# Performance work log

Hardware: AMD Instinct MI355X
Metric: run time of the kernel (lower is better)

Reference implementation:

```python
import jax, jax.numpy as jnp
import numpy as np

Q_MAX = 127.0  # 8-bit, narrow range [-127, 127] (pytorch-quantization default)


def fake_quant(x, amax):
    """Fake quantization with clipped-STE semantics (matches pytorch-quantization).

    amax may be a scalar (per-tensor) or broadcastable (per-channel). Treated as
    a constant (stop_gradient'd by caller where appropriate).
    """
    amax = jnp.maximum(amax, 1e-12)
    scale = amax / Q_MAX
    xq = jnp.round(jnp.clip(x / scale, -Q_MAX, Q_MAX)) * scale
    xc = jnp.clip(x, -amax, amax)  # identity grad inside range, zero outside
    return xc + jax.lax.stop_gradient(xq - xc)


def quant_conv1x1(x, w, b):
    """QuantConv2d with 1x1 kernel: fake-quant input (per-tensor dynamic max amax)
    and weight (per-output-channel max amax), then conv + bias.
    x: [B,C,H,W], w: [O,C], b: [O]
    """
    a_amax = jax.lax.stop_gradient(jnp.max(jnp.abs(x)))
    xq = fake_quant(x, a_amax)
    w_amax = jax.lax.stop_gradient(jnp.max(jnp.abs(w), axis=1, keepdims=True))
    wq = fake_quant(w, w_amax)
    y = jnp.einsum('bchw,oc->bohw', xq, wq)
    return y + b[None, :, None, None]


def setup_inputs() -> dict:
    key = jax.random.key(0)
    k1, k2, k3, k4 = jax.random.split(key, 4)
    B, C, Cr, H, W = 64, 32, 8, 128, 128
    x = jax.random.normal(k1, (B, C, H, W), dtype=jnp.float32)
    identity = jax.random.normal(k2, (B, C, H, W), dtype=jnp.float32)
    w_reduce = jax.random.normal(k3, (Cr, C), dtype=jnp.float32) * 0.1
    b_reduce = jnp.zeros((Cr,), dtype=jnp.float32)
    w_expand = jax.random.normal(k4, (C, Cr), dtype=jnp.float32) * 0.1
    b_expand = jnp.zeros((C,), dtype=jnp.float32)
    return {"x": x, "identity": identity,
            "w_reduce": w_reduce, "b_reduce": b_reduce,
            "w_expand": w_expand, "b_expand": b_expand}


def reference(x, identity, w_reduce, b_reduce, w_expand, b_expand):
    h = quant_conv1x1(x, w_reduce, b_reduce)      # [B,8,H,W]
    h = h * jax.nn.sigmoid(h)                     # SiLU
    g = quant_conv1x1(h, w_expand, b_expand)      # [B,32,H,W]
    return identity * jax.nn.sigmoid(g)
```

## Files before the change

kernel.cpp:

```cpp
#include <hip/hip_runtime.h>
#include <math.h>

#define QMAX 127.0f
#define CIN 32
#define CR 8
#define HW 16384
#define BATCH 64
#define NPIX (BATCH*HW)
#define NQUAD (NPIX/4)
#define NX (BATCH*CIN*HW)
#define COOP_BLOCKS (NQUAD/256)

#define H_OFF 64
#define WS_NEEDED ((size_t)(H_OFF + (size_t)NPIX * CR) * 4)

__device__ __forceinline__ float fq(float v, float inv_scale, float scale) {
    return rintf(fminf(fmaxf(v * inv_scale, -QMAX), QMAX)) * scale;
}
__device__ __forceinline__ float sigmoidf_(float v) {
    return __builtin_amdgcn_rcpf(1.0f + __expf(-v));
}

__device__ __forceinline__ void grid_bar(unsigned int* __restrict__ cnt,
                                         unsigned int* __restrict__ gen,
                                         unsigned int nb) {
    __syncthreads();
    if (threadIdx.x == 0) {
        unsigned int g = __hip_atomic_load(gen, __ATOMIC_RELAXED, __HIP_MEMORY_SCOPE_AGENT);
        unsigned int a = __hip_atomic_fetch_add(cnt, 1u, __ATOMIC_ACQ_REL, __HIP_MEMORY_SCOPE_AGENT);
        if (a == nb - 1u) {
            __hip_atomic_store(cnt, 0u, __ATOMIC_RELAXED, __HIP_MEMORY_SCOPE_AGENT);
            __hip_atomic_fetch_add(gen, 1u, __ATOMIC_RELEASE, __HIP_MEMORY_SCOPE_AGENT);
        } else {
            while (__hip_atomic_load(gen, __ATOMIC_RELAXED, __HIP_MEMORY_SCOPE_AGENT) == g)
                __builtin_amdgcn_s_sleep(1);
            __builtin_amdgcn_fence(__ATOMIC_ACQUIRE, "agent");
        }
    }
    __syncthreads();
}

__global__ __launch_bounds__(256, 4) void se_fused(const float* __restrict__ x,
                                                   const float* __restrict__ identity,
                                                   const float* __restrict__ wr,
                                                   const float* __restrict__ br,
                                                   const float* __restrict__ we,
                                                   const float* __restrict__ be,
                                                   unsigned int* __restrict__ wsu,
                                                   float* __restrict__ out) {
    int t = threadIdx.x;
    __shared__ float wqr[CR * CIN], wqe[CIN * CR], bsh[CR], besh[CIN], amr[CR], ame[CIN];
    __shared__ float red[4];

    if (t < CR) {
        float mm = 0.f;
        for (int c = 0; c < CIN; c++) mm = fmaxf(mm, fabsf(wr[t * CIN + c]));
        amr[t] = fmaxf(mm, 1e-12f);
        bsh[t] = br[t];
    }
    if (t >= 64 && t < 64 + CIN) {
        int r = t - 64;
        float mm = 0.f;
        for (int c = 0; c < CR; c++) mm = fmaxf(mm, fabsf(we[r * CR + c]));
        ame[r] = fmaxf(mm, 1e-12f);
        besh[r] = be[r];
    }
    __syncthreads();
    {
        float a1 = amr[t >> 5];
        wqr[t] = fq(wr[t], QMAX / a1, a1 * (1.f / QMAX));
        float a2 = ame[t >> 3];
        wqe[t] = fq(we[t], QMAX / a2, a2 * (1.f / QMAX));
    }
    __syncthreads();

    const int tid = blockIdx.x * 256 + t;

    {
        const float4* x4 = (const float4*)x;
        float m = 0.f;
#pragma unroll 8
        for (int i = 0; i < 32; i++) {
            float4 v = x4[tid + i * NQUAD];
            m = fmaxf(m, fmaxf(fmaxf(fabsf(v.x), fabsf(v.y)), fmaxf(fabsf(v.z), fabsf(v.w))));
        }
#pragma unroll
        for (int off = 32; off > 0; off >>= 1) m = fmaxf(m, __shfl_xor(m, off, 64));
        if ((t & 63) == 0) red[t >> 6] = m;
        __syncthreads();
        if (t == 0) {
            m = fmaxf(fmaxf(red[0], red[1]), fmaxf(red[2], red[3]));
            atomicMax(&wsu[0], __float_as_uint(m));
        }
    }
    grid_bar(&wsu[2], &wsu[3], COOP_BLOCKS);

    float a_amax = fmaxf(__uint_as_float(
        __hip_atomic_load(&wsu[0], __ATOMIC_ACQUIRE, __HIP_MEMORY_SCOPE_AGENT)), 1e-12f);
    float ascale = a_amax * (1.f / QMAX), ainv = QMAX / a_amax;
    const int b = tid >> 12;
    const int hw = (tid & 4095) << 2;
    const size_t base = (size_t)b * CIN * HW + hw;
    float h[CR][4];
    {
        float hacc[CR][4];
#pragma unroll
        for (int o = 0; o < CR; o++)
#pragma unroll
            for (int v = 0; v < 4; v++) hacc[o][v] = 0.f;
        const float* xb = x + base;
#pragma unroll
        for (int c = 0; c < CIN; c++) {
            float4 xv = *(const float4*)(xb + (size_t)c * HW);
            float q0 = fq(xv.x, ainv, ascale), q1 = fq(xv.y, ainv, ascale);
            float q2 = fq(xv.z, ainv, ascale), q3 = fq(xv.w, ainv, ascale);
#pragma unroll
            for (int o = 0; o < CR; o++) {
                float w = wqr[o * CIN + c];
                hacc[o][0] += q0 * w; hacc[o][1] += q1 * w;
                hacc[o][2] += q2 * w; hacc[o][3] += q3 * w;
            }
        }
        float m = 0.f;
#pragma unroll
        for (int o = 0; o < CR; o++) {
            float bb = bsh[o];
#pragma unroll
            for (int v = 0; v < 4; v++) {
                float hv = hacc[o][v] + bb;
                hv = hv * sigmoidf_(hv);
                h[o][v] = hv;
                m = fmaxf(m, fabsf(hv));
            }
        }
#pragma unroll
        for (int off = 32; off > 0; off >>= 1) m = fmaxf(m, __shfl_xor(m, off, 64));
        __syncthreads();
        if ((t & 63) == 0) red[t >> 6] = m;
        __syncthreads();
        if (t == 0) {
            m = fmaxf(fmaxf(red[0], red[1]), fmaxf(red[2], red[3]));
            atomicMax(&wsu[1], __float_as_uint(m));
        }
    }
    grid_bar(&wsu[2], &wsu[3], COOP_BLOCKS);

    float h_amax = fmaxf(__uint_as_float(
        __hip_atomic_load(&wsu[1], __ATOMIC_ACQUIRE, __HIP_MEMORY_SCOPE_AGENT)), 1e-12f);
    float hscale = h_amax * (1.f / QMAX), hinv = QMAX / h_amax;
#pragma unroll
    for (int o = 0; o < CR; o++)
#pragma unroll
        for (int v = 0; v < 4; v++) h[o][v] = fq(h[o][v], hinv, hscale);

#pragma unroll 4
    for (int o2 = 0; o2 < CIN; o2++) {
        float g0 = besh[o2], g1 = g0, g2 = g0, g3 = g0;
#pragma unroll
        for (int cr = 0; cr < CR; cr++) {
            float w = wqe[o2 * CR + cr];
            g0 += h[cr][0] * w; g1 += h[cr][1] * w;
            g2 += h[cr][2] * w; g3 += h[cr][3] * w;
        }
        size_t off = base + (size_t)o2 * HW;
        float4 idv = *(const float4*)(identity + off);
        float4 ov;
        ov.x = idv.x * sigmoidf_(g0);
        ov.y = idv.y * sigmoidf_(g1);
        ov.z = idv.z * sigmoidf_(g2);
        ov.w = idv.w * sigmoidf_(g3);
        *(float4*)(out + off) = ov;
    }
}

__global__ __launch_bounds__(256) void k1_xmax(const float4* __restrict__ x4,
                                               unsigned int* __restrict__ wsu) {
    int idx = blockIdx.x * 256 + threadIdx.x;
    float m = 0.f;
#pragma unroll
    for (int i = 0; i < 16; i++) {
        float4 v = x4[idx + i * 524288];
        m = fmaxf(m, fmaxf(fmaxf(fabsf(v.x), fabsf(v.y)), fmaxf(fabsf(v.z), fabsf(v.w))));
    }
#pragma unroll
    for (int off = 32; off > 0; off >>= 1) m = fmaxf(m, __shfl_xor(m, off, 64));
    __shared__ float red[4];
    int t = threadIdx.x;
    if ((t & 63) == 0) red[t >> 6] = m;
    __syncthreads();
    if (t == 0) {
        m = fmaxf(fmaxf(red[0], red[1]), fmaxf(red[2], red[3]));
        atomicMax(&wsu[0], __float_as_uint(m));
    }
}

__global__ __launch_bounds__(256) void k2_hmax(const float* __restrict__ x,
                                               const float* __restrict__ wr,
                                               const float* __restrict__ br,
                                               const unsigned int* __restrict__ wsu,
                                               unsigned int* __restrict__ hmax,
                                               float* __restrict__ hbuf) {
    __shared__ float wq[CR * CIN], bsh[CR], amr[CR];
    int t = threadIdx.x;
    if (t < CR) {
        float mm = 0.f;
        for (int c = 0; c < CIN; c++) mm = fmaxf(mm, fabsf(wr[t * CIN + c]));
        amr[t] = fmaxf(mm, 1e-12f);
        bsh[t] = br[t];
    }
    __syncthreads();
    {
        float amax = amr[t >> 5];
        wq[t] = fq(wr[t], QMAX / amax, amax * (1.f / QMAX));
    }
    __syncthreads();
    float a_amax = fmaxf(__uint_as_float(wsu[0]), 1e-12f);
    float scale = a_amax * (1.f / QMAX), inv_scale = QMAX / a_amax;
    int tid = blockIdx.x * 256 + t;
    int b = tid >> 12;
    int hw = (tid & 4095) << 2;
    const float* xb = x + (size_t)b * CIN * HW + hw;
    float hacc[CR][4];
#pragma unroll
    for (int o = 0; o < CR; o++)
#pragma unroll
        for (int v = 0; v < 4; v++) hacc[o][v] = 0.f;
#pragma unroll
    for (int c = 0; c < CIN; c++) {
        float4 xv = *(const float4*)(xb + (size_t)c * HW);
        float q0 = fq(xv.x, inv_scale, scale), q1 = fq(xv.y, inv_scale, scale);
        float q2 = fq(xv.z, inv_scale, scale), q3 = fq(xv.w, inv_scale, scale);
#pragma unroll
        for (int o = 0; o < CR; o++) {
            float w = wq[o * CIN + c];
            hacc[o][0] += q0 * w; hacc[o][1] += q1 * w;
            hacc[o][2] += q2 * w; hacc[o][3] += q3 * w;
        }
    }
    float m = 0.f;
#pragma unroll
    for (int o = 0; o < CR; o++) {
        float bb = bsh[o];
        float4 hv;
        float* hp = (float*)&hv;
#pragma unroll
        for (int v = 0; v < 4; v++) {
            float h = hacc[o][v] + bb;
            h = h * sigmoidf_(h);
            hp[v] = h;
            m = fmaxf(m, fabsf(h));
        }
        if (hbuf) *(float4*)(hbuf + ((size_t)(b * CR + o)) * HW + hw) = hv;
    }
#pragma unroll
    for (int off = 32; off > 0; off >>= 1) m = fmaxf(m, __shfl_xor(m, off, 64));
    __shared__ float red[4];
    if ((t & 63) == 0) red[t >> 6] = m;
    __syncthreads();
    if (t == 0) {
        m = fmaxf(fmaxf(red[0], red[1]), fmaxf(red[2], red[3]));
        atomicMax(hmax, __float_as_uint(m));
    }
}

__global__ __launch_bounds__(256) void k3_out(const float* __restrict__ hbuf,
                                              const float* __restrict__ identity,
                                              const float* __restrict__ we,
                                              const float* __restrict__ be,
                                              const unsigned int* __restrict__ wsu,
                                              float* __restrict__ out) {
    const int y = blockIdx.y;
    __shared__ float wqe[16 * CR], besh[16], ame[16];
    int t = threadIdx.x;
    if (t < 16) {
        int r = 16 * y + t;
        float mm = 0.f;
        for (int c = 0; c < CR; c++) mm = fmaxf(mm, fabsf(we[r * CR + c]));
        ame[t] = fmaxf(mm, 1e-12f);
        besh[t] = be[r];
    }
    __syncthreads();
    if (t < 128) {
        int r16 = t >> 3;
        float amax = ame[r16];
        wqe[t] = fq(we[(16 * y + r16) * CR + (t & 7)], QMAX / amax, amax * (1.f / QMAX));
    }
    __syncthreads();
    float h_amax = fmaxf(__uint_as_float(wsu[1]), 1e-12f);
    float hscale = h_amax * (1.f / QMAX), hinv = QMAX / h_amax;
    int tid = blockIdx.x * 256 + t;
    int b = tid >> 12;
    int hw = (tid & 4095) << 2;
    size_t base = (size_t)b * CIN * HW + hw;
    float hq[CR][4];
#pragma unroll
    for (int cr = 0; cr < CR; cr++) {
        float4 hv = *(const float4*)(hbuf + ((size_t)(b * CR + cr)) * HW + hw);
        hq[cr][0] = fq(hv.x, hinv, hscale);
        hq[cr][1] = fq(hv.y, hinv, hscale);
        hq[cr][2] = fq(hv.z, hinv, hscale);
        hq[cr][3] = fq(hv.w, hinv, hscale);
    }
#pragma unroll 4
    for (int o = 0; o < 16; o++) {
        float g0 = besh[o], g1 = g0, g2 = g0, g3 = g0;
#pragma unroll
        for (int cr = 0; cr < CR; cr++) {
            float w = wqe[o * CR + cr];
            g0 += hq[cr][0] * w; g1 += hq[cr][1] * w;
            g2 += hq[cr][2] * w; g3 += hq[cr][3] * w;
        }
        size_t off = base + (size_t)(16 * y + o) * HW;
        float4 idv = *(const float4*)(identity + off);
        float4 ov;
        ov.x = idv.x * sigmoidf_(g0);
        ov.y = idv.y * sigmoidf_(g1);
        ov.z = idv.z * sigmoidf_(g2);
        ov.w = idv.w * sigmoidf_(g3);
        *(float4*)(out + off) = ov;
    }
}

__global__ __launch_bounds__(256) void k3_out_rc(const float* __restrict__ x,
                                                 const float* __restrict__ identity,
                                                 const float* __restrict__ wr,
                                                 const float* __restrict__ br,
                                                 const float* __restrict__ we,
                                                 const float* __restrict__ be,
                                                 const unsigned int* __restrict__ wsu,
                                                 float* __restrict__ out) {
    __shared__ float wqr[CR * CIN], wqe[CIN * CR], bsh[CR], besh[CIN], amr[CR], ame[CIN];
    int t = threadIdx.x;
    if (t < CR) {
        float mm = 0.f;
        for (int c = 0; c < CIN; c++) mm = fmaxf(mm, fabsf(wr[t * CIN + c]));
        amr[t] = fmaxf(mm, 1e-12f);
        bsh[t] = br[t];
    }
    if (t >= 64 && t < 64 + CIN) {
        int r = t - 64;
        float mm = 0.f;
        for (int c = 0; c < CR; c++) mm = fmaxf(mm, fabsf(we[r * CR + c]));
        ame[r] = fmaxf(mm, 1e-12f);
        besh[r] = be[r];
    }
    __syncthreads();
    {
        float amax = amr[t >> 5];
        wqr[t] = fq(wr[t], QMAX / amax, amax * (1.f / QMAX));
        float amax2 = ame[t >> 3];
        wqe[t] = fq(we[t], QMAX / amax2, amax2 * (1.f / QMAX));
    }
    __syncthreads();
    float a_amax = fmaxf(__uint_as_float(wsu[0]), 1e-12f);
    float ascale = a_amax * (1.f / QMAX), ainv = QMAX / a_amax;
    float h_amax = fmaxf(__uint_as_float(wsu[1]), 1e-12f);
    float hscale = h_amax * (1.f / QMAX), hinv = QMAX / h_amax;
    int tid = blockIdx.x * 256 + t;
    int b = tid >> 12;
    int hw = (tid & 4095) << 2;
    size_t base = (size_t)b * CIN * HW + hw;
    const float* xb = x + base;
    float hq[CR][4];
    {
        float hacc[CR][4];
#pragma unroll
        for (int o = 0; o < CR; o++)
#pragma unroll
            for (int v = 0; v < 4; v++) hacc[o][v] = 0.f;
#pragma unroll
        for (int c = 0; c < CIN; c++) {
            float4 xv = *(const float4*)(xb + (size_t)c * HW);
            float q0 = fq(xv.x, ainv, ascale), q1 = fq(xv.y, ainv, ascale);
            float q2 = fq(xv.z, ainv, ascale), q3 = fq(xv.w, ainv, ascale);
#pragma unroll
            for (int o = 0; o < CR; o++) {
                float w = wqr[o * CIN + c];
                hacc[o][0] += q0 * w; hacc[o][1] += q1 * w;
                hacc[o][2] += q2 * w; hacc[o][3] += q3 * w;
            }
        }
#pragma unroll
        for (int o = 0; o < CR; o++) {
            float bb = bsh[o];
#pragma unroll
            for (int v = 0; v < 4; v++) {
                float h = hacc[o][v] + bb;
                h = h * sigmoidf_(h);
                hq[o][v] = fq(h, hinv, hscale);
            }
        }
    }
#pragma unroll 4
    for (int o2 = 0; o2 < CIN; o2++) {
        float g0 = besh[o2], g1 = g0, g2 = g0, g3 = g0;
#pragma unroll
        for (int cr = 0; cr < CR; cr++) {
            float w = wqe[o2 * CR + cr];
            g0 += hq[cr][0] * w; g1 += hq[cr][1] * w;
            g2 += hq[cr][2] * w; g3 += hq[cr][3] * w;
        }
        size_t off = base + (size_t)o2 * HW;
        float4 idv = *(const float4*)(identity + off);
        float4 ov;
        ov.x = idv.x * sigmoidf_(g0);
        ov.y = idv.y * sigmoidf_(g1);
        ov.z = idv.z * sigmoidf_(g2);
        ov.w = idv.w * sigmoidf_(g3);
        *(float4*)(out + off) = ov;
    }
}

extern "C" void kernel_launch(void* const* d_in, const int* in_sizes, int n_in,
                              void* d_out, int out_size, void* d_ws, size_t ws_size,
                              hipStream_t stream) {
    const float* x        = (const float*)d_in[0];
    const float* identity = (const float*)d_in[1];
    const float* wr       = (const float*)d_in[2];
    const float* br       = (const float*)d_in[3];
    const float* we       = (const float*)d_in[4];
    const float* be       = (const float*)d_in[5];
    float* out            = (float*)d_out;
    float* wsf            = (float*)d_ws;
    unsigned int* wsu     = (unsigned int*)d_ws;

    hipMemsetAsync(d_ws, 0, 16, stream);

    int maxb = 0;
    hipError_t qerr = hipOccupancyMaxActiveBlocksPerMultiprocessor(&maxb, se_fused, 256, 0);
    bool coop_ok = false;
    if (qerr == hipSuccess && maxb >= 4) {
        void* args[] = {(void*)&x, (void*)&identity, (void*)&wr, (void*)&br,
                        (void*)&we, (void*)&be, (void*)&wsu, (void*)&out};
        hipError_t lerr = hipLaunchCooperativeKernel((void*)se_fused, dim3(COOP_BLOCKS),
                                                     dim3(256), args, 0, stream);
        coop_ok = (lerr == hipSuccess);
    }
    if (coop_ok) return;

    const bool big_ws = (ws_size >= WS_NEEDED);
    float* hbuf = big_ws ? (wsf + H_OFF) : nullptr;
    hipLaunchKernelGGL(k1_xmax, dim3(2048), dim3(256), 0, stream, (const float4*)x, wsu);
    hipLaunchKernelGGL(k2_hmax, dim3(NQUAD / 256), dim3(256), 0, stream,
                       x, wr, br, wsu, &wsu[1], hbuf);
    if (big_ws) {
        hipLaunchKernelGGL(k3_out, dim3(NQUAD / 256, 2), dim3(256), 0, stream,
                           hbuf, identity, we, be, wsu, out);
    } else {
        hipLaunchKernelGGL(k3_out_rc, dim3(NQUAD / 256), dim3(256), 0, stream,
                           x, identity, wr, br, we, be, wsu, out);
    }
}
```

Before: 374.9 us.

## Launch fused kernel normally and batch channel loads for memory-level parallelism

Replaces the cooperative launch of the fused grid-barrier kernel with a plain launch, which removes cooperative launch overhead but relies on all 1024 blocks being co-resident without any guarantee (deadlock risk if they are not). It also restructures the input and identity channel loops to issue eight float4 loads up front before computing, aiming to raise outstanding memory requests. The barrier's initial generation load is tightened to acquire ordering.

Measured after the change: 371.6 us. About the same (-0.9%).

```diff
diff --git a/kernel.cpp b/kernel.cpp
--- a/kernel.cpp
+++ b/kernel.cpp
@@ -26,7 +26,7 @@
                                          unsigned int nb) {
     __syncthreads();
     if (threadIdx.x == 0) {
-        unsigned int g = __hip_atomic_load(gen, __ATOMIC_RELAXED, __HIP_MEMORY_SCOPE_AGENT);
+        unsigned int g = __hip_atomic_load(gen, __ATOMIC_ACQUIRE, __HIP_MEMORY_SCOPE_AGENT);
         unsigned int a = __hip_atomic_fetch_add(cnt, 1u, __ATOMIC_ACQ_REL, __HIP_MEMORY_SCOPE_AGENT);
         if (a == nb - 1u) {
             __hip_atomic_store(cnt, 0u, __ATOMIC_RELAXED, __HIP_MEMORY_SCOPE_AGENT);
@@ -109,16 +109,22 @@
 #pragma unroll
             for (int v = 0; v < 4; v++) hacc[o][v] = 0.f;
         const float* xb = x + base;
-#pragma unroll
-        for (int c = 0; c < CIN; c++) {
-            float4 xv = *(const float4*)(xb + (size_t)c * HW);
-            float q0 = fq(xv.x, ainv, ascale), q1 = fq(xv.y, ainv, ascale);
-            float q2 = fq(xv.z, ainv, ascale), q3 = fq(xv.w, ainv, ascale);
-#pragma unroll
-            for (int o = 0; o < CR; o++) {
-                float w = wqr[o * CIN + c];
-                hacc[o][0] += q0 * w; hacc[o][1] += q1 * w;
-                hacc[o][2] += q2 * w; hacc[o][3] += q3 * w;
+        for (int cg_ = 0; cg_ < CIN / 8; cg_++) {
+            float4 xv[8];
+#pragma unroll
+            for (int j = 0; j < 8; j++)
+                xv[j] = *(const float4*)(xb + (size_t)(cg_ * 8 + j) * HW);
+#pragma unroll
+            for (int j = 0; j < 8; j++) {
+                int c = cg_ * 8 + j;
+                float q0 = fq(xv[j].x, ainv, ascale), q1 = fq(xv[j].y, ainv, ascale);
+                float q2 = fq(xv[j].z, ainv, ascale), q3 = fq(xv[j].w, ainv, ascale);
+#pragma unroll
+                for (int o = 0; o < CR; o++) {
+                    float w = wqr[o * CIN + c];
+                    hacc[o][0] += q0 * w; hacc[o][1] += q1 * w;
+                    hacc[o][2] += q2 * w; hacc[o][3] += q3 * w;
+                }
             }
         }
         float m = 0.f;
@@ -153,23 +159,29 @@
 #pragma unroll
         for (int v = 0; v < 4; v++) h[o][v] = fq(h[o][v], hinv, hscale);
 
-#pragma unroll 4
-    for (int o2 = 0; o2 < CIN; o2++) {
-        float g0 = besh[o2], g1 = g0, g2 = g0, g3 = g0;
-#pragma unroll
-        for (int cr = 0; cr < CR; cr++) {
-            float w = wqe[o2 * CR + cr];
-            g0 += h[cr][0] * w; g1 += h[cr][1] * w;
-            g2 += h[cr][2] * w; g3 += h[cr][3] * w;
-        }
-        size_t off = base + (size_t)o2 * HW;
-        float4 idv = *(const float4*)(identity + off);
-        float4 ov;
-        ov.x = idv.x * sigmoidf_(g0);
-        ov.y = idv.y * sigmoidf_(g1);
-        ov.z = idv.z * sigmoidf_(g2);
-        ov.w = idv.w * sigmoidf_(g3);
-        *(float4*)(out + off) = ov;
+    for (int og = 0; og < CIN / 8; og++) {
+        float4 idv[8];
+#pragma unroll
+        for (int j = 0; j < 8; j++)
+            idv[j] = *(const float4*)(identity + base + (size_t)(og * 8 + j) * HW);
+#pragma unroll
+        for (int j = 0; j < 8; j++) {
+            int o2 = og * 8 + j;
+            float g0 = besh[o2], g1 = g0, g2 = g0, g3 = g0;
+#pragma unroll
+            for (int cr = 0; cr < CR; cr++) {
+                float w = wqe[o2 * CR + cr];
+                g0 += h[cr][0] * w; g1 += h[cr][1] * w;
+                g2 += h[cr][2] * w; g3 += h[cr][3] * w;
+            }
+            size_t off = base + (size_t)o2 * HW;
+            float4 ov;
+            ov.x = idv[j].x * sigmoidf_(g0);
+            ov.y = idv[j].y * sigmoidf_(g1);
+            ov.z = idv[j].z * sigmoidf_(g2);
+            ov.w = idv[j].w * sigmoidf_(g3);
+            *(float4*)(out + off) = ov;
+        }
     }
 }
 
@@ -428,15 +440,11 @@
 
     int maxb = 0;
     hipError_t qerr = hipOccupancyMaxActiveBlocksPerMultiprocessor(&maxb, se_fused, 256, 0);
-    bool coop_ok = false;
     if (qerr == hipSuccess && maxb >= 4) {
-        void* args[] = {(void*)&x, (void*)&identity, (void*)&wr, (void*)&br,
-                        (void*)&we, (void*)&be, (void*)&wsu, (void*)&out};
-        hipError_t lerr = hipLaunchCooperativeKernel((void*)se_fused, dim3(COOP_BLOCKS),
-                                                     dim3(256), args, 0, stream);
-        coop_ok = (lerr == hipSuccess);
-    }
-    if (coop_ok) return;
+        hipLaunchKernelGGL(se_fused, dim3(COOP_BLOCKS), dim3(256), 0, stream,
+                           x, identity, wr, br, we, be, wsu, out);
+        return;
+    }
 
     const bool big_ws = (ws_size >= WS_NEEDED);
     float* hbuf = big_ws ? (wsf + H_OFF) : nullptr;
```
